# Optimization experiments

Measured on AMD Instinct MI355X. Metric: run time of the kernel, lower is better.

The kernel has to match this reference:

```python
import jax, jax.numpy as jnp
import numpy as np

N = 100000   # nodes
E = 1600000  # edges
H = 64       # hidden_dim
NT = 512     # num_taxo
TD = 32      # taxo_dim
ID = 32      # item_dim
L = 2        # taxo_layers
ETA = 0.5
SLOPE = 0.01  # leaky_relu default


def setup_inputs() -> dict:
    key = jax.random.key(0)
    ks = jax.random.split(key, 20)
    p = lambda i, shape, s: jax.random.normal(ks[i], shape, dtype=jnp.float32) * s
    return {
        'h': p(0, (N, H), 1.0),
        'src': jax.random.randint(ks[1], (E,), 0, N),
        'dst': jax.random.randint(ks[2], (E,), 0, N),
        'taxo_cats': jax.random.randint(ks[3], (N, L), 0, NT),
        'idx_rows': jnp.arange(N),
        'idx_cols': jax.random.randint(ks[4], (N,), 0, N),
        'idx_vals': jax.random.uniform(ks[5], (N,), dtype=jnp.float32),
        'norm_rows': jnp.arange(N),
        'norm_cols': jax.random.randint(ks[6], (N,), 0, N),
        'norm_vals': jax.random.uniform(ks[7], (N,), dtype=jnp.float32),
        'W_w': p(8, (H, H), H ** -0.5),
        'W_b': jnp.zeros((H,), jnp.float32),
        'prelu_a': jnp.full((1,), 0.25, jnp.float32),
        'taxo_mean': p(9, (NT, H), 0.1),
        'taxo_std_log': p(10, (NT, H), 0.1),
        'conv_wh': p(11, (1, 2 * H), (2 * H) ** -0.5),
        'conv_Ww': p(12, (H, H), H ** -0.5),
        'conv_Wb': jnp.zeros((H,), jnp.float32),
        'psi_W': p(13, (1, H, H), H ** -0.5),
        'psi_b': jnp.zeros((1,), jnp.float32),
        'mlp_w0': p(14, (TD, H), H ** -0.5),
        'mlp_b0': jnp.zeros((TD,), jnp.float32),
        'mlp_w1': p(15, (TD, H), H ** -0.5),
        'mlp_b1': jnp.zeros((TD,), jnp.float32),
        'mlp_w2': p(16, (ID, H), H ** -0.5),
        'mlp_b2': jnp.zeros((ID,), jnp.float32),
    }


def _spmm(rows, cols, vals, x, nrows):
    # sparse COO [nrows, n] @ dense [n, d]
    return jax.ops.segment_sum(vals[:, None] * x[cols], rows, num_segments=nrows)


def _edge_softmax(scores, dst, n):
    # softmax of edge scores grouped by destination node
    m = jax.ops.segment_max(scores, dst, num_segments=n)
    e = jnp.exp(scores - m[dst])
    s = jax.ops.segment_sum(e, dst, num_segments=n)
    return e / s[dst]


def _prelu(x, a):
    return jnp.where(x >= 0, x, a * x)


def _normalize(x):
    return x / jnp.maximum(jnp.linalg.norm(x, axis=1, keepdims=True), 1e-12)


def _conv(h, tax, src, dst, wh, Ww, Wb):
    hs = h[src]  # [E,H]
    wf = jnp.concatenate([hs, h[dst]], axis=1) @ wh.T  # [E,1]
    wf = jnp.where(wf >= 0, wf, SLOPE * wf)
    alpha_f = _edge_softmax(wf, dst, N)
    wt = jnp.sum(tax[src] * tax[dst], axis=1, keepdims=True)  # [E,1]
    alpha_t = _edge_softmax(wt, dst, N)
    alpha = ETA * alpha_f + (1.0 - ETA) * alpha_t
    z = jax.ops.segment_sum(hs * alpha, dst, num_segments=N)  # u_mul_e + sum
    return z @ Ww.T + Wb


def reference(h, src, dst, taxo_cats, idx_rows, idx_cols, idx_vals,
              norm_rows, norm_cols, norm_vals, W_w, W_b, prelu_a,
              taxo_mean, taxo_std_log, conv_wh, conv_Ww, conv_Wb,
              psi_W, psi_b, mlp_w0, mlp_b0, mlp_w1, mlp_b1, mlp_w2, mlp_b2):
    h = _prelu(h @ W_w.T + W_b, prelu_a)
    means = taxo_mean[taxo_cats]            # [N,L,H]
    stds = jnp.exp(taxo_std_log[taxo_cats])  # [N,L,H]
    tax = _spmm(norm_rows, norm_cols, norm_vals, means.reshape(N, L * H), N)
    # conv layers share the SAME weights (ModuleList([ConvLayer]*num_layer))
    for i in range(2):
        h = _conv(h, tax, src, dst, conv_wh, conv_Ww, conv_Wb)
        if i < 1:
            h = _prelu(h, prelu_a)
    raw = h
    emb_h = _normalize(h @ mlp_w2.T + mlp_b2)
    embs = []
    for i, (w, b) in enumerate([(mlp_w0, mlp_b0), (mlp_w1, mlp_b1)]):
        h_rev = _spmm(idx_rows, idx_cols, idx_vals, h, N)
        mi = means[:, i]
        si = stds[:, i]
        stpl = jnp.einsum('bi,ij,bj->b', h_rev, psi_W[0], mi)[:, None] + psi_b
        tau = jax.nn.sigmoid(stpl) * jnp.exp(-si)
        cur = (1.0 - tau) * h_rev + tau * mi
        cur = _spmm(norm_rows, norm_cols, norm_vals, cur, N)
        embs.append(_normalize(cur @ w.T + b))
    emb = jnp.stack(embs, axis=2).reshape(N, -1)
    emb = jnp.concatenate([emb_h, emb], axis=1)  # [N, out_dim]
    return raw, emb
```

## Files before the change

kernel.cpp:

```cpp
#include <hip/hip_runtime.h>

constexpr int H  = 64;
constexpr int NT = 512;
constexpr int NBMAX = 512;

#define FMA4(acc_, s_, v_) { (acc_).x += (s_)*(v_).x; (acc_).y += (s_)*(v_).y; \
                             (acc_).z += (s_)*(v_).z; (acc_).w += (s_)*(v_).w; }

__global__ void k_gram(const float* __restrict__ tm, float* __restrict__ G) {
    int idx = blockIdx.x * blockDim.x + threadIdx.x;
    if (idx >= NT * NT) return;
    int a = idx >> 9, b = idx & (NT - 1);
    const float* ra = tm + a * H;
    const float* rb = tm + b * H;
    float s = 0.f;
#pragma unroll
    for (int k = 0; k < H; ++k) s += ra[k] * rb[k];
    G[idx] = s;
}

__global__ void k_wt(const float* __restrict__ Ww, const float* __restrict__ Wc,
                     const float* __restrict__ w2,
                     float* __restrict__ WTw, float* __restrict__ WTc,
                     float* __restrict__ WT2) {
    int i = blockIdx.x * 256 + threadIdx.x;
    if (i < 64 * 64) {
        int j = i >> 6, l = i & 63;
        WTw[l * 64 + j] = Ww[i];
        WTc[l * 64 + j] = Wc[i];
        if (j < 32) WT2[l * 32 + j] = w2[i & 2047];
    }
}

__global__ void k_phist(const int* __restrict__ dst, int* __restrict__ histT,
                        const int* __restrict__ ncols, const int* __restrict__ cats,
                        const float* __restrict__ nvals, uint2* __restrict__ nm,
                        int NB, int NPB, int CH, int E, int N) {
    __shared__ int hist[NBMAX];
    int b = blockIdx.x, t = threadIdx.x;
    int gid = b * 256 + t;
    if (gid < N) {
        int j = ncols[gid];
        nm[gid] = make_uint2(__float_as_uint(nvals[gid]),
                             (unsigned)(cats[j * 2] | (cats[j * 2 + 1] << 16)));
    }
    for (int i = t; i < NB; i += 256) hist[i] = 0;
    __syncthreads();
    int e0 = b * CH, e1 = min(E, e0 + CH);
    for (int e = e0 + t; e < e1; e += 256)
        atomicAdd(&hist[dst[e] >> 8], 1);
    __syncthreads();
    for (int i = t; i < NB; i += 256) histT[i * NPB + b] = hist[i];
}

__global__ void k_btot(const int* __restrict__ histT, int* __restrict__ tot, int NPB) {
    __shared__ int sh[256];
    int bk = blockIdx.x, t = threadIdx.x;
    int s = 0;
    for (int j = t; j < NPB; j += 256) s += histT[bk * NPB + j];
    sh[t] = s;
    __syncthreads();
    for (int o = 128; o; o >>= 1) { if (t < o) sh[t] += sh[t + o]; __syncthreads(); }
    if (!t) tot[bk] = sh[0];
}

__global__ void k_bscan(const int* __restrict__ tot, int* __restrict__ bbase,
                        int* __restrict__ row_start, int NB, int N, int E) {
    __shared__ int sh[NBMAX];
    int t = threadIdx.x;
    int v = (t < NB) ? tot[t] : 0;
    sh[t] = v;
    __syncthreads();
    for (int o = 1; o < NBMAX; o <<= 1) {
        int x = (t >= o) ? sh[t - o] : 0;
        __syncthreads();
        sh[t] += x;
        __syncthreads();
    }
    if (t < NB) bbase[t] = sh[t] - v;
    if (t == 0) { bbase[NB] = E; row_start[N] = E; }
}

__global__ void k_boff(const int* __restrict__ histT, const int* __restrict__ bbase,
                       int* __restrict__ boff, int NPB) {
    __shared__ int sh[NBMAX];
    int bk = blockIdx.x, t = threadIdx.x;
    int v = (t < NPB) ? histT[bk * NPB + t] : 0;
    sh[t] = v;
    __syncthreads();
    for (int o = 1; o < NBMAX; o <<= 1) {
        int x = (t >= o) ? sh[t - o] : 0;
        __syncthreads();
        sh[t] += x;
        __syncthreads();
    }
    if (t < NPB) boff[bk * NPB + t] = bbase[bk] + sh[t] - v;
}

__global__ void k_part(const int* __restrict__ src, const int* __restrict__ dst,
                       const int* __restrict__ boff, unsigned* __restrict__ brec,
                       int NB, int NPB, int CH, int E) {
    __shared__ int cur[NBMAX];
    int b = blockIdx.x, t = threadIdx.x;
    for (int i = t; i < NB; i += 256) cur[i] = boff[i * NPB + b];
    __syncthreads();
    int e0 = b * CH, e1 = min(E, e0 + CH);
    for (int e = e0 + t; e < e1; e += 256) {
        int s = src[e], d = dst[e];
        int pos = atomicAdd(&cur[d >> 8], 1);
        brec[pos] = (unsigned)s | ((unsigned)(d & 255) << 24);
    }
}

__global__ void k_csr(const unsigned* __restrict__ brec, const int* __restrict__ bbase,
                      const uint2* __restrict__ nm, const float* __restrict__ G,
                      int* __restrict__ row_start, int* __restrict__ src_s,
                      float* __restrict__ et, float* __restrict__ sumt, int N) {
    __shared__ int   sdeg[256];
    __shared__ int   scur[256];
    __shared__ float ssum[256];
    __shared__ float snv[256];
    __shared__ int   scc[256];
    int b = blockIdx.x, t = threadIdx.x;
    int node0 = b << 8;
    int ebase = bbase[b], eend = bbase[b + 1];
    sdeg[t] = 0; scur[t] = 0; ssum[t] = 0.f;
    int n = node0 + t;
    if (n < N) { uint2 m = nm[n]; snv[t] = __uint_as_float(m.x); scc[t] = (int)m.y; }
    __syncthreads();
    for (int i = ebase + t; i < eend; i += 256)
        atomicAdd(&sdeg[brec[i] >> 24], 1);
    __syncthreads();
    int val = sdeg[t];
    for (int o = 1; o < 256; o <<= 1) {
        int x = (t >= o) ? sdeg[t - o] : 0;
        __syncthreads();
        sdeg[t] += x;
        __syncthreads();
    }
    int gstart = ebase + sdeg[t] - val;
    if (n < N) row_start[n] = gstart;
    sdeg[t] = gstart;
    __syncthreads();
    for (int i = ebase + t; i < eend; i += 256) {
        unsigned r = brec[i];
        int s = (int)(r & 0xFFFFFFu);
        int j = (int)(r >> 24);
        int c = atomicAdd(&scur[j], 1);
        int k = sdeg[j] + c;
        src_s[k] = s;
        uint2 ms = nm[s];
        float nvs = __uint_as_float(ms.x);
        int cs = (int)ms.y;
        int cd = scc[j];
        float wt = nvs * snv[j] *
                   (G[(cs & 0xffff) * NT + (cd & 0xffff)] + G[(cs >> 16) * NT + (cd >> 16)]);
        float ev = __expf(wt);
        et[k] = ev;
        atomicAdd(&ssum[j], ev);
    }
    __syncthreads();
    if (n < N) sumt[n] = ssum[t];
}

#define LDH(S) (*reinterpret_cast<const float4*>(h_in + (size_t)(S) * H + f))
template <bool PRELU, bool SUV, bool EMBH>
__global__ void __launch_bounds__(256, 8)
k_aggt(const float* __restrict__ h_in, const int* __restrict__ src_s,
       const int* __restrict__ row_start, const float* __restrict__ et,
       const float* __restrict__ sumt, const float* __restrict__ s_u,
       const float* __restrict__ s_v,
       const float* __restrict__ WT, const float* __restrict__ b,
       const float* __restrict__ a_ptr, const float* __restrict__ wh,
       float* __restrict__ s_u_o, float* __restrict__ s_v_o,
       const float* __restrict__ WT2, const float* __restrict__ b2,
       float* __restrict__ emb_out,
       float* __restrict__ out, int N) {
    __shared__ float WF[64 * 64];
    __shared__ float xs[4][4][64];
    int t = threadIdx.x;
    for (int i = t; i < 64 * 64; i += 256) WF[i] = WT[i];
    __syncthreads();
    int sg = t >> 4, l16 = t & 15, f = l16 * 4;
    int wid = t >> 6, g = sg & 3;
    int n = blockIdx.x * 16 + sg;

    float4 z = make_float4(0.f, 0.f, 0.f, 0.f);
    if (n < N) {
        int kb = row_start[n], ke = row_start[n + 1];
        if (ke > kb) {
            float sv = s_v[n];
            float invt = 0.5f / sumt[n];
            float ssf = 0.f;
            float4 zf0 = z, zf1 = z, zt0 = z, zt1 = z;
            for (int k0 = kb; k0 < ke; k0 += 16) {
                int cnt = ke - k0; cnt = cnt < 16 ? cnt : 16;
                int cl = cnt - 1;
                int myk = k0 + (l16 <= cl ? l16 : cl);
                int ms = src_s[myk];
                float me = et[myk] * invt;
                float mw = s_u[ms] + sv;
                mw = mw >= 0.f ? mw : 0.01f * mw;
                float mf = __expf(mw);
                if (l16 > cl) { mf = 0.f; me = 0.f; }
                ssf += mf;
                for (int j0 = 0; j0 < cnt; j0 += 4) {
                    int jB = min(j0 + 1, cl), jC = min(j0 + 2, cl), jD = min(j0 + 3, cl);
                    int sA = __shfl(ms, j0, 16), sB = __shfl(ms, jB, 16);
                    int sC = __shfl(ms, jC, 16), sD = __shfl(ms, jD, 16);
                    float tfA = __shfl(mf, j0, 16), tfB = __shfl(mf, jB, 16);
                    float tfC = __shfl(mf, jC, 16), tfD = __shfl(mf, jD, 16);
                    float teA = __shfl(me, j0, 16), teB = __shfl(me, jB, 16);
                    float teC = __shfl(me, jC, 16), teD = __shfl(me, jD, 16);
                    float fB = (j0 + 1 <= cl) ? tfB : 0.f;
                    float fC = (j0 + 2 <= cl) ? tfC : 0.f;
                    float fD = (j0 + 3 <= cl) ? tfD : 0.f;
                    float eB = (j0 + 1 <= cl) ? teB : 0.f;
                    float eC = (j0 + 2 <= cl) ? teC : 0.f;
                    float eD = (j0 + 3 <= cl) ? teD : 0.f;
                    const float4 hA = LDH(sA);
                    const float4 hB = LDH(sB);
                    const float4 hC = LDH(sC);
                    const float4 hD = LDH(sD);
                    FMA4(zf0, tfA, hA); FMA4(zt0, teA, hA);
                    FMA4(zf1, fB, hB);  FMA4(zt1, eB, hB);
                    FMA4(zf0, fC, hC);  FMA4(zt0, eC, hC);
                    FMA4(zf1, fD, hD);  FMA4(zt1, eD, hD);
                }
            }
            ssf += __shfl_xor(ssf, 1); ssf += __shfl_xor(ssf, 2);
            ssf += __shfl_xor(ssf, 4); ssf += __shfl_xor(ssf, 8);
            float invf = 0.5f / ssf;
            z.x = (zf0.x + zf1.x) * invf + (zt0.x + zt1.x);
            z.y = (zf0.y + zf1.y) * invf + (zt0.y + zt1.y);
            z.z = (zf0.z + zf1.z) * invf + (zt0.z + zt1.z);
            z.w = (zf0.w + zf1.w) * invf + (zt0.w + zt1.w);
        }
    }

    *reinterpret_cast<float4*>(&xs[wid][g][f]) = z;
    float a = PRELU ? a_ptr[0] : 0.f;
    float4 acc = *reinterpret_cast<const float4*>(b + f);
#pragma unroll 2
    for (int l0 = 0; l0 < 64; l0 += 4) {
        const float* wp = &WF[l0 * 64 + f];
        float4 wv0 = *reinterpret_cast<const float4*>(wp);
        float4 wv1 = *reinterpret_cast<const float4*>(wp + 64);
        float4 wv2 = *reinterpret_cast<const float4*>(wp + 128);
        float4 wv3 = *reinterpret_cast<const float4*>(wp + 192);
        float4 x4 = *reinterpret_cast<const float4*>(&xs[wid][g][l0]);
        FMA4(acc, x4.x, wv0); FMA4(acc, x4.y, wv1);
        FMA4(acc, x4.z, wv2); FMA4(acc, x4.w, wv3);
    }
    if constexpr (PRELU) {
        acc.x = acc.x >= 0.f ? acc.x : a * acc.x;
        acc.y = acc.y >= 0.f ? acc.y : a * acc.y;
        acc.z = acc.z >= 0.f ? acc.z : a * acc.z;
        acc.w = acc.w >= 0.f ? acc.w : a * acc.w;
    }
    if (n < N) *reinterpret_cast<float4*>(out + (size_t)n * H + f) = acc;
    if constexpr (SUV) {
        float4 wu = *reinterpret_cast<const float4*>(wh + f);
        float4 wv = *reinterpret_cast<const float4*>(wh + H + f);
        float u = acc.x * wu.x + acc.y * wu.y + acc.z * wu.z + acc.w * wu.w;
        float v = acc.x * wv.x + acc.y * wv.y + acc.z * wv.z + acc.w * wv.w;
        u += __shfl_xor(u, 1); v += __shfl_xor(v, 1);
        u += __shfl_xor(u, 2); v += __shfl_xor(v, 2);
        u += __shfl_xor(u, 4); v += __shfl_xor(v, 4);
        u += __shfl_xor(u, 8); v += __shfl_xor(v, 8);
        if (l16 == 0 && n < N) { s_u_o[n] = u; s_v_o[n] = v; }
    }
    if constexpr (EMBH) {
        *reinterpret_cast<float4*>(&xs[wid][g][f]) = acc;
        if (l16 < 8) {
            float4 e4 = *reinterpret_cast<const float4*>(b2 + f);
#pragma unroll 2
            for (int l0 = 0; l0 < 64; l0 += 4) {
                float4 x4 = *reinterpret_cast<const float4*>(&xs[wid][g][l0]);
                float4 u0 = *reinterpret_cast<const float4*>(WT2 + (l0 + 0) * 32 + f);
                float4 u1 = *reinterpret_cast<const float4*>(WT2 + (l0 + 1) * 32 + f);
                float4 u2 = *reinterpret_cast<const float4*>(WT2 + (l0 + 2) * 32 + f);
                float4 u3 = *reinterpret_cast<const float4*>(WT2 + (l0 + 3) * 32 + f);
                FMA4(e4, x4.x, u0); FMA4(e4, x4.y, u1);
                FMA4(e4, x4.z, u2); FMA4(e4, x4.w, u3);
            }
            float sq = e4.x * e4.x + e4.y * e4.y + e4.z * e4.z + e4.w * e4.w;
            sq += __shfl_xor(sq, 1);
            sq += __shfl_xor(sq, 2);
            sq += __shfl_xor(sq, 4);
            float invn = 1.f / fmaxf(sqrtf(sq), 1e-12f);
            e4.x *= invn; e4.y *= invn; e4.z *= invn; e4.w *= invn;
            if (n < N) *reinterpret_cast<float4*>(emb_out + (size_t)n * 96 + f) = e4;
        }
    }
}

template <bool PRELU, bool SUV>
__global__ void __launch_bounds__(256, 4)
k_trans(const float* __restrict__ in, const float* __restrict__ WT,
        const float* __restrict__ b, const float* __restrict__ a_ptr,
        const float* __restrict__ wh,
        float* __restrict__ s_u_o, float* __restrict__ s_v_o,
        float* __restrict__ out, int N) {
    __shared__ float WF[64 * 64];
    __shared__ float xs[4][8][68];
    int t = threadIdx.x;
    for (int i = t; i < 64 * 64; i += 256) WF[i] = WT[i];
    __syncthreads();
    int wid = t >> 6, lane = t & 63;
    int g = lane >> 4, f = lane & 15;
    float a = PRELU ? a_ptr[0] : 0.f;
    float4 bias = *reinterpret_cast<const float4*>(b + 4 * f);
    int n0 = blockIdx.x * 32 + wid * 8 + g;
    int n1 = n0 + 4;
    float4 xv0 = make_float4(0.f, 0.f, 0.f, 0.f), xv1 = xv0;
    if (n0 < N) xv0 = *reinterpret_cast<const float4*>(in + (size_t)n0 * H + 4 * f);
    if (n1 < N) xv1 = *reinterpret_cast<const float4*>(in + (size_t)n1 * H + 4 * f);
    *reinterpret_cast<float4*>(&xs[wid][g][4 * f])     = xv0;
    *reinterpret_cast<float4*>(&xs[wid][4 + g][4 * f]) = xv1;
    float4 accP = make_float4(0.f, 0.f, 0.f, 0.f), accQ = accP;
#pragma unroll 2
    for (int l0 = 0; l0 < 64; l0 += 4) {
        const float* wp = &WF[l0 * 64 + 4 * f];
        float4 wv0 = *reinterpret_cast<const float4*>(wp);
        float4 wv1 = *reinterpret_cast<const float4*>(wp + 64);
        float4 wv2 = *reinterpret_cast<const float4*>(wp + 128);
        float4 wv3 = *reinterpret_cast<const float4*>(wp + 192);
        float4 xP = *reinterpret_cast<const float4*>(&xs[wid][g][l0]);
        float4 xQ = *reinterpret_cast<const float4*>(&xs[wid][4 + g][l0]);
        FMA4(accP, xP.x, wv0); FMA4(accP, xP.y, wv1);
        FMA4(accP, xP.z, wv2); FMA4(accP, xP.w, wv3);
        FMA4(accQ, xQ.x, wv0); FMA4(accQ, xQ.y, wv1);
        FMA4(accQ, xQ.z, wv2); FMA4(accQ, xQ.w, wv3);
    }
    auto epi = [&](float4 acc, int n) {
        acc.x += bias.x; acc.y += bias.y; acc.z += bias.z; acc.w += bias.w;
        if constexpr (PRELU) {
            acc.x = acc.x >= 0.f ? acc.x : a * acc.x;
            acc.y = acc.y >= 0.f ? acc.y : a * acc.y;
            acc.z = acc.z >= 0.f ? acc.z : a * acc.z;
            acc.w = acc.w >= 0.f ? acc.w : a * acc.w;
        }
        if (n < N) *reinterpret_cast<float4*>(out + (size_t)n * H + 4 * f) = acc;
        if constexpr (SUV) {
            float4 wu = *reinterpret_cast<const float4*>(wh + 4 * f);
            float4 wv = *reinterpret_cast<const float4*>(wh + H + 4 * f);
            float u = acc.x * wu.x + acc.y * wu.y + acc.z * wu.z + acc.w * wu.w;
            float v = acc.x * wv.x + acc.y * wv.y + acc.z * wv.z + acc.w * wv.w;
            u += __shfl_xor(u, 1); v += __shfl_xor(v, 1);
            u += __shfl_xor(u, 2); v += __shfl_xor(v, 2);
            u += __shfl_xor(u, 4); v += __shfl_xor(v, 4);
            u += __shfl_xor(u, 8); v += __shfl_xor(v, 8);
            if (f == 0 && n < N) { s_u_o[n] = u; s_v_o[n] = v; }
        }
    };
    epi(accP, n0);
    epi(accQ, n1);
}

__global__ void __launch_bounds__(256, 4)
k_post1(const float* __restrict__ raw, const int* __restrict__ icols,
        const float* __restrict__ ivals, const float* __restrict__ Psi,
        const float* __restrict__ psib, const int* __restrict__ cats,
        const float* __restrict__ tm, const float* __restrict__ tsl,
        float* __restrict__ cur0, float* __restrict__ cur1, int N) {
    __shared__ float PF[64 * 68];
    __shared__ float xs[4][8][68];
    int t = threadIdx.x;
    for (int i = t; i < 64 * 64; i += 256) { int l = i >> 6, j = i & 63; PF[l * 68 + j] = Psi[i]; }
    __syncthreads();
    int wid = t >> 6, lane = t & 63;
    int g = lane >> 4, f = lane & 15;
    float pb = psib[0];
    int n0 = blockIdx.x * 32 + wid * 8 + g;
    int n1 = n0 + 4;
    float4 hr0 = make_float4(0.f, 0.f, 0.f, 0.f), hr1 = hr0;
    if (n0 < N) {
        int c = icols[n0]; float iv = ivals[n0];
        float4 rv = *reinterpret_cast<const float4*>(raw + (size_t)c * H + 4 * f);
        hr0.x = iv * rv.x; hr0.y = iv * rv.y; hr0.z = iv * rv.z; hr0.w = iv * rv.w;
    }
    if (n1 < N) {
        int c = icols[n1]; float iv = ivals[n1];
        float4 rv = *reinterpret_cast<const float4*>(raw + (size_t)c * H + 4 * f);
        hr1.x = iv * rv.x; hr1.y = iv * rv.y; hr1.z = iv * rv.z; hr1.w = iv * rv.w;
    }
    *reinterpret_cast<float4*>(&xs[wid][g][4 * f])     = hr0;
    *reinterpret_cast<float4*>(&xs[wid][4 + g][4 * f]) = hr1;
    float4 v0 = make_float4(0.f, 0.f, 0.f, 0.f), v1 = v0;
#pragma unroll 2
    for (int l0 = 0; l0 < 64; l0 += 4) {
        const float* pp = &PF[l0 * 68 + 4 * f];
        float4 pv0 = *reinterpret_cast<const float4*>(pp);
        float4 pv1 = *reinterpret_cast<const float4*>(pp + 68);
        float4 pv2 = *reinterpret_cast<const float4*>(pp + 136);
        float4 pv3 = *reinterpret_cast<const float4*>(pp + 204);
        float4 xP = *reinterpret_cast<const float4*>(&xs[wid][g][l0]);
        float4 xQ = *reinterpret_cast<const float4*>(&xs[wid][4 + g][l0]);
        FMA4(v0, xP.x, pv0); FMA4(v0, xP.y, pv1); FMA4(v0, xP.z, pv2); FMA4(v0, xP.w, pv3);
        FMA4(v1, xQ.x, pv0); FMA4(v1, xQ.y, pv1); FMA4(v1, xQ.z, pv2); FMA4(v1, xQ.w, pv3);
    }
    auto epi = [&](float4 v, float4 hr, int n) {
        if (n >= N) return;
#pragma unroll
        for (int i2 = 0; i2 < 2; ++i2) {
            int c = cats[n * 2 + i2];
            float4 m4 = *reinterpret_cast<const float4*>(tm + (size_t)c * H + 4 * f);
            float sd = v.x * m4.x + v.y * m4.y + v.z * m4.z + v.w * m4.w;
            sd += __shfl_xor(sd, 1);
            sd += __shfl_xor(sd, 2);
            sd += __shfl_xor(sd, 4);
            sd += __shfl_xor(sd, 8);
            float sig = 1.f / (1.f + __expf(-(sd + pb)));
            float4 t4 = *reinterpret_cast<const float4*>(tsl + (size_t)c * H + 4 * f);
            float4 tau, cv;
            tau.x = sig * __expf(-__expf(t4.x));
            tau.y = sig * __expf(-__expf(t4.y));
            tau.z = sig * __expf(-__expf(t4.z));
            tau.w = sig * __expf(-__expf(t4.w));
            cv.x = (1.f - tau.x) * hr.x + tau.x * m4.x;
            cv.y = (1.f - tau.y) * hr.y + tau.y * m4.y;
            cv.z = (1.f - tau.z) * hr.z + tau.z * m4.z;
            cv.w = (1.f - tau.w) * hr.w + tau.w * m4.w;
            *reinterpret_cast<float4*>((i2 ? cur1 : cur0) + (size_t)n * H + 4 * f) = cv;
        }
    };
    epi(v0, hr0, n0);
    epi(v1, hr1, n1);
}

__global__ void __launch_bounds__(256, 4)
k_post2(const float* __restrict__ cur0, const float* __restrict__ cur1,
        const int* __restrict__ ncols, const float* __restrict__ nvals,
        const float* __restrict__ w0, const float* __restrict__ b0,
        const float* __restrict__ w1, const float* __restrict__ b1,
        float* __restrict__ emb_out, int N) {
    __shared__ float WC[64 * 68];
    __shared__ float xs[4][4][2][68];
    int t = threadIdx.x;
    for (int i = t; i < 64 * 64; i += 256) {
        int j = i >> 6, l = i & 63;
        WC[l * 68 + j] = (j < 32) ? w0[j * 64 + l] : w1[(j - 32) * 64 + l];
    }
    __syncthreads();
    int wid = t >> 6, lane = t & 63;
    int g = lane >> 4, f = lane & 15;
    int half = f >> 3;
    const float* bb = half ? b1 : b0;
    float4 bias = *reinterpret_cast<const float4*>(bb + 4 * (f & 7));
    for (int it = 0; it < 2; ++it) {
        int n = blockIdx.x * 32 + wid * 8 + it * 4 + g;
        float4 x0 = make_float4(0.f, 0.f, 0.f, 0.f), x1 = x0;
        if (n < N) {
            int c = ncols[n];
            float gsc = nvals[n];
            float4 c0v = *reinterpret_cast<const float4*>(cur0 + (size_t)c * H + 4 * f);
            float4 c1v = *reinterpret_cast<const float4*>(cur1 + (size_t)c * H + 4 * f);
            x0.x = gsc * c0v.x; x0.y = gsc * c0v.y; x0.z = gsc * c0v.z; x0.w = gsc * c0v.w;
            x1.x = gsc * c1v.x; x1.y = gsc * c1v.y; x1.z = gsc * c1v.z; x1.w = gsc * c1v.w;
        }
        *reinterpret_cast<float4*>(&xs[wid][g][0][4 * f]) = x0;
        *reinterpret_cast<float4*>(&xs[wid][g][1][4 * f]) = x1;
        float4 acc = bias;
#pragma unroll 4
        for (int l0 = 0; l0 < 64; l0 += 4) {
            float4 x4  = *reinterpret_cast<const float4*>(&xs[wid][g][half][l0]);
            float4 wv0 = *reinterpret_cast<const float4*>(&WC[(l0 + 0) * 68 + 4 * f]);
            float4 wv1 = *reinterpret_cast<const float4*>(&WC[(l0 + 1) * 68 + 4 * f]);
            float4 wv2 = *reinterpret_cast<const float4*>(&WC[(l0 + 2) * 68 + 4 * f]);
            float4 wv3 = *reinterpret_cast<const float4*>(&WC[(l0 + 3) * 68 + 4 * f]);
            FMA4(acc, x4.x, wv0); FMA4(acc, x4.y, wv1);
            FMA4(acc, x4.z, wv2); FMA4(acc, x4.w, wv3);
        }
        float sq = acc.x * acc.x + acc.y * acc.y + acc.z * acc.z + acc.w * acc.w;
        sq += __shfl_xor(sq, 1);
        sq += __shfl_xor(sq, 2);
        sq += __shfl_xor(sq, 4);
        float invn = 1.f / fmaxf(sqrtf(sq), 1e-12f);
        if (n < N) {
            int jb = (f & 7) * 4;
            float* o = emb_out + (size_t)n * 96 + 32 + half;
            o[2 * (jb + 0)] = acc.x * invn;
            o[2 * (jb + 1)] = acc.y * invn;
            o[2 * (jb + 2)] = acc.z * invn;
            o[2 * (jb + 3)] = acc.w * invn;
        }
    }
}

extern "C" void kernel_launch(void* const* d_in, const int* in_sizes, int n_in,
                              void* d_out, int out_size, void* d_ws, size_t ws_size,
                              hipStream_t stream) {
    const float* h      = (const float*)d_in[0];
    const int*   src    = (const int*)d_in[1];
    const int*   dst    = (const int*)d_in[2];
    const int*   cats   = (const int*)d_in[3];
    const int*   icols  = (const int*)d_in[5];
    const float* ivals  = (const float*)d_in[6];
    const int*   ncols  = (const int*)d_in[8];
    const float* nvals  = (const float*)d_in[9];
    const float* W_w    = (const float*)d_in[10];
    const float* W_b    = (const float*)d_in[11];
    const float* pre_a  = (const float*)d_in[12];
    const float* tm     = (const float*)d_in[13];
    const float* tsl    = (const float*)d_in[14];
    const float* wh     = (const float*)d_in[15];
    const float* cWw    = (const float*)d_in[16];
    const float* cWb    = (const float*)d_in[17];
    const float* psiW   = (const float*)d_in[18];
    const float* psib   = (const float*)d_in[19];
    const float* w0     = (const float*)d_in[20];
    const float* b0     = (const float*)d_in[21];
    const float* w1     = (const float*)d_in[22];
    const float* b1     = (const float*)d_in[23];
    const float* w2     = (const float*)d_in[24];
    const float* b2     = (const float*)d_in[25];

    const int N = in_sizes[0] / H;
    const int E = in_sizes[1];
    const int NB = (N + 255) >> 8;
    const int NPB = NB;
    const int CH = (E + NPB - 1) / NPB;

    char* ws = (char*)d_ws;
    size_t off = 0;
    auto alloc = [&](size_t bytes) -> void* {
        void* p = ws + off;
        off = (off + bytes + 255) & ~(size_t)255;
        return p;
    };
    float*    A        = (float*)   alloc((size_t)N * H * 4);
    float*    B        = (float*)   alloc((size_t)N * H * 4);
    float*    et       = (float*)   alloc((size_t)E * 4);
    int*      src_s    = (int*)     alloc((size_t)E * 4);
    unsigned* brec     = (unsigned*)alloc((size_t)E * 4);
    uint2*    nm       = (uint2*)   alloc((size_t)N * 8);
    int*      row_start= (int*)     alloc((size_t)(N + 1) * 4);
    float*    sumt     = (float*)   alloc((size_t)N * 4);
    float*    s_u0     = (float*)   alloc((size_t)N * 4);
    float*    s_v0     = (float*)   alloc((size_t)N * 4);
    float*    s_u1     = (float*)   alloc((size_t)N * 4);
    float*    s_v1     = (float*)   alloc((size_t)N * 4);
    float*    G        = (float*)   alloc((size_t)NT * NT * 4);
    int*      histT    = (int*)     alloc((size_t)NB * NPB * 4);
    int*      boff     = (int*)     alloc((size_t)NB * NPB * 4);
    int*      tot      = (int*)     alloc((size_t)NB * 4);
    int*      bbase    = (int*)     alloc((size_t)(NB + 1) * 4);
    float*    WTw      = (float*)   alloc(64 * 64 * 4);
    float*    WTc      = (float*)   alloc(64 * 64 * 4);
    float*    WT2      = (float*)   alloc(64 * 32 * 4);
    (void)ws_size; (void)n_in; (void)out_size;

    float* rawOut  = (float*)d_out;
    float* emb_out = (float*)d_out + (size_t)N * H;

    dim3 b256(256);
    int nb16 = (N + 15) / 16;
    int nb32 = (N + 31) / 32;

    k_wt<<<16, b256, 0, stream>>>(W_w, cWw, w2, WTw, WTc, WT2);
    k_gram<<<(NT * NT + 255) / 256, b256, 0, stream>>>(tm, G);
    k_phist<<<NPB, b256, 0, stream>>>(dst, histT, ncols, cats, nvals, nm,
                                      NB, NPB, CH, E, N);
    k_btot<<<NB, b256, 0, stream>>>(histT, tot, NPB);
    k_bscan<<<1, NBMAX, 0, stream>>>(tot, bbase, row_start, NB, N, E);
    k_boff<<<NB, NBMAX, 0, stream>>>(histT, bbase, boff, NPB);
    k_part<<<NPB, b256, 0, stream>>>(src, dst, boff, brec, NB, NPB, CH, E);
    k_csr<<<NB, b256, 0, stream>>>(brec, bbase, nm, G, row_start, src_s, et, sumt, N);

    k_trans<true, true><<<nb32, b256, 0, stream>>>(
        h, WTw, W_b, pre_a, wh, s_u0, s_v0, A, N);

    k_aggt<true, true, false><<<nb16, b256, 0, stream>>>(
        A, src_s, row_start, et, sumt, s_u0, s_v0,
        WTc, cWb, pre_a, wh, s_u1, s_v1, nullptr, nullptr, nullptr, B, N);

    k_aggt<false, false, true><<<nb16, b256, 0, stream>>>(
        B, src_s, row_start, et, sumt, s_u1, s_v1,
        WTc, cWb, pre_a, nullptr, nullptr, nullptr, WT2, b2, emb_out, rawOut, N);

    k_post1<<<nb32, b256, 0, stream>>>(rawOut, icols, ivals, psiW, psib, cats, tm, tsl,
                                       A, B, N);
    k_post2<<<nb32, b256, 0, stream>>>(A, B, ncols, nvals, w0, b0, w1, b1, emb_out, N);
}
```

Baseline: 347.3 us.

## Pack edge source and weight into uint2, swizzle shared tile, stage emb weights in LDS

The CSR build now writes the sorted source index and the edge exp-weight as one interleaved uint2 array, so each aggregation lane fetches both with a single 8-byte load instead of two separate streams. The shared staging buffer for node features is XOR-swizzled by group to reduce LDS bank conflicts. In the final conv pass, the emb_h projection weights are copied into shared memory and all 16 lanes compute two output columns each, replacing the previous scheme where 8 lanes read weights from global memory. This costs extra LDS per block in the EMBH variant, which may lower occupancy.

```diff
diff --git a/kernel.cpp b/kernel.cpp
--- a/kernel.cpp
+++ b/kernel.cpp
@@ -114,8 +114,8 @@
 
 __global__ void k_csr(const unsigned* __restrict__ brec, const int* __restrict__ bbase,
                       const uint2* __restrict__ nm, const float* __restrict__ G,
-                      int* __restrict__ row_start, int* __restrict__ src_s,
-                      float* __restrict__ et, float* __restrict__ sumt, int N) {
+                      int* __restrict__ row_start, uint2* __restrict__ se,
+                      float* __restrict__ sumt, int N) {
     __shared__ int   sdeg[256];
     __shared__ int   scur[256];
     __shared__ float ssum[256];
@@ -148,7 +148,6 @@
         int j = (int)(r >> 24);
         int c = atomicAdd(&scur[j], 1);
         int k = sdeg[j] + c;
-        src_s[k] = s;
         uint2 ms = nm[s];
         float nvs = __uint_as_float(ms.x);
         int cs = (int)ms.y;
@@ -156,7 +155,7 @@
         float wt = nvs * snv[j] *
                    (G[(cs & 0xffff) * NT + (cd & 0xffff)] + G[(cs >> 16) * NT + (cd >> 16)]);
         float ev = __expf(wt);
-        et[k] = ev;
+        se[k] = make_uint2((unsigned)s, __float_as_uint(ev));
         atomicAdd(&ssum[j], ev);
     }
     __syncthreads();
@@ -166,8 +165,8 @@
 #define LDH(S) (*reinterpret_cast<const float4*>(h_in + (size_t)(S) * H + f))
 template <bool PRELU, bool SUV, bool EMBH>
 __global__ void __launch_bounds__(256, 8)
-k_aggt(const float* __restrict__ h_in, const int* __restrict__ src_s,
-       const int* __restrict__ row_start, const float* __restrict__ et,
+k_aggt(const float* __restrict__ h_in, const uint2* __restrict__ se,
+       const int* __restrict__ row_start,
        const float* __restrict__ sumt, const float* __restrict__ s_u,
        const float* __restrict__ s_v,
        const float* __restrict__ WT, const float* __restrict__ b,
@@ -177,12 +176,17 @@
        float* __restrict__ emb_out,
        float* __restrict__ out, int N) {
     __shared__ float WF[64 * 64];
-    __shared__ float xs[4][4][64];
+    __shared__ float W2S[EMBH ? 64 * 32 : 1];
+    __shared__ float xs[4][256];
     int t = threadIdx.x;
     for (int i = t; i < 64 * 64; i += 256) WF[i] = WT[i];
+    if constexpr (EMBH) {
+        for (int i = t; i < 64 * 32; i += 256) W2S[i] = WT2[i];
+    }
     __syncthreads();
     int sg = t >> 4, l16 = t & 15, f = l16 * 4;
     int wid = t >> 6, g = sg & 3;
+    int gsw = g << 2;
     int n = blockIdx.x * 16 + sg;
 
     float4 z = make_float4(0.f, 0.f, 0.f, 0.f);
@@ -197,8 +201,9 @@
                 int cnt = ke - k0; cnt = cnt < 16 ? cnt : 16;
                 int cl = cnt - 1;
                 int myk = k0 + (l16 <= cl ? l16 : cl);
-                int ms = src_s[myk];
-                float me = et[myk] * invt;
+                uint2 p = se[myk];
+                int ms = (int)p.x;
+                float me = __uint_as_float(p.y) * invt;
                 float mw = s_u[ms] + sv;
                 mw = mw >= 0.f ? mw : 0.01f * mw;
                 float mf = __expf(mw);
@@ -238,7 +243,7 @@
         }
     }
 
-    *reinterpret_cast<float4*>(&xs[wid][g][f]) = z;
+    *reinterpret_cast<float4*>(&xs[wid][(g << 6) | (f ^ gsw)]) = z;
     float a = PRELU ? a_ptr[0] : 0.f;
     float4 acc = *reinterpret_cast<const float4*>(b + f);
 #pragma unroll 2
@@ -248,7 +253,7 @@
         float4 wv1 = *reinterpret_cast<const float4*>(wp + 64);
         float4 wv2 = *reinterpret_cast<const float4*>(wp + 128);
         float4 wv3 = *reinterpret_cast<const float4*>(wp + 192);
-        float4 x4 = *reinterpret_cast<const float4*>(&xs[wid][g][l0]);
+        float4 x4 = *reinterpret_cast<const float4*>(&xs[wid][(g << 6) | (l0 ^ gsw)]);
         FMA4(acc, x4.x, wv0); FMA4(acc, x4.y, wv1);
         FMA4(acc, x4.z, wv2); FMA4(acc, x4.w, wv3);
     }
@@ -271,26 +276,30 @@
         if (l16 == 0 && n < N) { s_u_o[n] = u; s_v_o[n] = v; }
     }
     if constexpr (EMBH) {
-        *reinterpret_cast<float4*>(&xs[wid][g][f]) = acc;
-        if (l16 < 8) {
-            float4 e4 = *reinterpret_cast<const float4*>(b2 + f);
+        *reinterpret_cast<float4*>(&xs[wid][(g << 6) | (f ^ gsw)]) = acc;
+        int c0 = 2 * l16;
+        float2 bb2 = *reinterpret_cast<const float2*>(b2 + c0);
+        float e0 = bb2.x, e1 = bb2.y;
 #pragma unroll 2
-            for (int l0 = 0; l0 < 64; l0 += 4) {
-                float4 x4 = *reinterpret_cast<const float4*>(&xs[wid][g][l0]);
-                float4 u0 = *reinterpret_cast<const float4*>(WT2 + (l0 + 0) * 32 + f);
-                float4 u1 = *reinterpret_cast<const float4*>(WT2 + (l0 + 1) * 32 + f);
-                float4 u2 = *reinterpret_cast<const float4*>(WT2 + (l0 + 2) * 32 + f);
-                float4 u3 = *reinterpret_cast<const float4*>(WT2 + (l0 + 3) * 32 + f);
-                FMA4(e4, x4.x, u0); FMA4(e4, x4.y, u1);
-                FMA4(e4, x4.z, u2); FMA4(e4, x4.w, u3);
-            }
-            float sq = e4.x * e4.x + e4.y * e4.y + e4.z * e4.z + e4.w * e4.w;
-            sq += __shfl_xor(sq, 1);
-            sq += __shfl_xor(sq, 2);
-            sq += __shfl_xor(sq, 4);
-            float invn = 1.f / fmaxf(sqrtf(sq), 1e-12f);
-            e4.x *= invn; e4.y *= invn; e4.z *= invn; e4.w *= invn;
-            if (n < N) *reinterpret_cast<float4*>(emb_out + (size_t)n * 96 + f) = e4;
+        for (int l0 = 0; l0 < 64; l0 += 4) {
+            float4 x4 = *reinterpret_cast<const float4*>(&xs[wid][(g << 6) | (l0 ^ gsw)]);
+            const float* wp = &W2S[l0 * 32 + c0];
+            float2 w0v = *reinterpret_cast<const float2*>(wp);
+            float2 w1v = *reinterpret_cast<const float2*>(wp + 32);
+            float2 w2v = *reinterpret_cast<const float2*>(wp + 64);
+            float2 w3v = *reinterpret_cast<const float2*>(wp + 96);
+            e0 += x4.x * w0v.x + x4.y * w1v.x + x4.z * w2v.x + x4.w * w3v.x;
+            e1 += x4.x * w0v.y + x4.y * w1v.y + x4.z * w2v.y + x4.w * w3v.y;
+        }
+        float sq = e0 * e0 + e1 * e1;
+        sq += __shfl_xor(sq, 1);
+        sq += __shfl_xor(sq, 2);
+        sq += __shfl_xor(sq, 4);
+        sq += __shfl_xor(sq, 8);
+        float invn = 1.f / fmaxf(sqrtf(sq), 1e-12f);
+        if (n < N) {
+            *reinterpret_cast<float2*>(emb_out + (size_t)n * 96 + c0) =
+                make_float2(e0 * invn, e1 * invn);
         }
     }
 }
@@ -531,8 +540,7 @@
     };
     float*    A        = (float*)   alloc((size_t)N * H * 4);
     float*    B        = (float*)   alloc((size_t)N * H * 4);
-    float*    et       = (float*)   alloc((size_t)E * 4);
-    int*      src_s    = (int*)     alloc((size_t)E * 4);
+    uint2*    se       = (uint2*)   alloc((size_t)E * 8);
     unsigned* brec     = (unsigned*)alloc((size_t)E * 4);
     uint2*    nm       = (uint2*)   alloc((size_t)N * 8);
     int*      row_start= (int*)     alloc((size_t)(N + 1) * 4);
@@ -566,17 +574,17 @@
     k_bscan<<<1, NBMAX, 0, stream>>>(tot, bbase, row_start, NB, N, E);
     k_boff<<<NB, NBMAX, 0, stream>>>(histT, bbase, boff, NPB);
     k_part<<<NPB, b256, 0, stream>>>(src, dst, boff, brec, NB, NPB, CH, E);
-    k_csr<<<NB, b256, 0, stream>>>(brec, bbase, nm, G, row_start, src_s, et, sumt, N);
+    k_csr<<<NB, b256, 0, stream>>>(brec, bbase, nm, G, row_start, se, sumt, N);
 
     k_trans<true, true><<<nb32, b256, 0, stream>>>(
         h, WTw, W_b, pre_a, wh, s_u0, s_v0, A, N);
 
     k_aggt<true, true, false><<<nb16, b256, 0, stream>>>(
-        A, src_s, row_start, et, sumt, s_u0, s_v0,
+        A, se, row_start, sumt, s_u0, s_v0,
         WTc, cWb, pre_a, wh, s_u1, s_v1, nullptr, nullptr, nullptr, B, N);
 
     k_aggt<false, false, true><<<nb16, b256, 0, stream>>>(
-        B, src_s, row_start, et, sumt, s_u1, s_v1,
+        B, se, row_start, sumt, s_u1, s_v1,
         WTc, cWb, pre_a, nullptr, nullptr, nullptr, WT2, b2, emb_out, rawOut, N);
 
     k_post1<<<nb32, b256, 0, stream>>>(rawOut, icols, ivals, psiW, psib, cats, tm, tsl,
```

Result: faster. 327.3 us (-5.7%).
